# Kernel optimization log

Measured on AMD Instinct MI355X. Metric: run time of the kernel, lower is better.

Reference implementation:

```python
import jax, jax.numpy as jnp
import numpy as np

DIM = 1152
HEADS = 9
MID = 256
B, N = 8, 1024


def _conprefix(x, dw, db, uw, ub):
    # torch Linear: y = x @ W.T + b
    kv = jnp.tanh(x @ dw.T + db) @ uw.T + ub  # [B, N, 2*dim]
    q = jnp.zeros(kv.shape[:2] + (DIM,), kv.dtype)
    return jnp.concatenate([q, kv], axis=-1)  # [B, N, 3*dim]


def setup_inputs() -> dict:
    key = jax.random.key(0)
    ks = jax.random.split(key, 12)
    s = 0.02
    return {
        "x": jax.random.normal(ks[0], (B, N, DIM), dtype=jnp.float32),
        "Wqkv": jax.random.normal(ks[1], (3 * DIM, DIM), dtype=jnp.float32) * s,
        "Wproj": jax.random.normal(ks[2], (DIM, DIM), dtype=jnp.float32) * s,
        "bproj": jax.random.normal(ks[3], (DIM,), dtype=jnp.float32) * s,
        "down_w": jax.random.normal(ks[4], (MID, DIM), dtype=jnp.float32) * s,
        "down_b": jax.random.normal(ks[5], (MID,), dtype=jnp.float32) * s,
        "up_w": jax.random.normal(ks[6], (2 * DIM, MID), dtype=jnp.float32) * s,
        "up_b": jax.random.normal(ks[7], (2 * DIM,), dtype=jnp.float32) * s,
        "pdown_w": jax.random.normal(ks[8], (MID, DIM), dtype=jnp.float32) * s,
        "pdown_b": jax.random.normal(ks[9], (MID,), dtype=jnp.float32) * s,
        "pup_w": jax.random.normal(ks[10], (2 * DIM, MID), dtype=jnp.float32) * s,
        "pup_b": jax.random.normal(ks[11], (2 * DIM,), dtype=jnp.float32) * s,
        "task": 5,
    }


def reference(x, Wqkv, Wproj, bproj, down_w, down_b, up_w, up_b,
              pdown_w, pdown_b, pup_w, pup_b, task):
    b, n, c = x.shape
    hd = c // HEADS
    scale = hd ** (-0.5)
    qkv = x @ Wqkv.T  # [B, N, 3C] (qkv_bias=False)
    task_prefix_tensor = None
    if task <= 3:
        pass
    elif task == 4:
        qkv = qkv + _conprefix(x, down_w, down_b, up_w, up_b)
        task_prefix_tensor = down_w
    else:
        qkv = (qkv + _conprefix(x, pdown_w, pdown_b, pup_w, pup_b)
                   + _conprefix(x, down_w, down_b, up_w, up_b))
        task_prefix_tensor = down_w
    qkv = qkv.reshape(b, n, 3, HEADS, hd).transpose(2, 0, 3, 1, 4)  # [3,B,H,N,hd]
    q, k, v = qkv[0], qkv[1], qkv[2]
    attn = jax.nn.softmax(jnp.einsum('bhqd,bhkd->bhqk', q, k) * scale, axis=-1)
    out = jnp.einsum('bhqk,bhkd->bhqd', attn, v)  # [B,H,N,hd]
    out = out.transpose(0, 2, 1, 3).reshape(b, n, c)
    out = out @ Wproj.T + bproj
    return (out, task_prefix_tensor)
```

## Files before the change

kernel.cpp:

```cpp
#include <hip/hip_runtime.h>
#include <math.h>

namespace {

typedef unsigned short u16;
typedef __attribute__((ext_vector_type(8))) short short8;
typedef __attribute__((ext_vector_type(4))) float f32x4;
typedef __attribute__((ext_vector_type(16))) float f32x16;

constexpr int kDim   = 1152;
constexpr int kHeads = 9;
constexpr int kMid   = 256;
constexpr int kB     = 8;
constexpr int kN     = 1024;
constexpr int kM     = kB * kN;
constexpr int kQS    = 3584;
constexpr float kCexp  = 0.12753837360881433f;

__device__ __forceinline__ u16 f2bf(float f) {
    unsigned u = __builtin_bit_cast(unsigned, f);
    return (u16)((u + 0x7FFFu + ((u >> 16) & 1u)) >> 16);
}
__device__ __forceinline__ float bf2f(u16 h) {
    unsigned u = ((unsigned)h) << 16;
    return __builtin_bit_cast(float, u);
}

__device__ __forceinline__ void gload_lds16(const void* g, void* l) {
    __builtin_amdgcn_global_load_lds(
        (const __attribute__((address_space(1))) unsigned int*)g,
        (__attribute__((address_space(3))) unsigned int*)l,
        16, 0, 0);
}

__device__ __forceinline__ unsigned cvtpk(float a, float b) {
    unsigned r;
    asm volatile("v_cvt_pk_bf16_f32 %0, %1, %2" : "=v"(r) : "v"(a), "v"(b));
    return r;
}

__device__ __forceinline__ void halfswap(unsigned& x, unsigned& y, bool hihalf) {
    const unsigned xs = (unsigned)__shfl_xor((int)x, 32);
    const unsigned ys = (unsigned)__shfl_xor((int)y, 32);
    const unsigned nx = hihalf ? ys : x;
    const unsigned ny = hihalf ? y : xs;
    x = nx; y = ny;
}

__device__ __forceinline__ short8 build_pfrag(float p0, float p1, float p2, float p3,
                                              float p4, float p5, float p6, float p7,
                                              bool hihalf) {
    unsigned x1 = cvtpk(p0, p1), y1 = cvtpk(p4, p5);
    unsigned x2 = cvtpk(p2, p3), y2 = cvtpk(p6, p7);
    halfswap(x1, y1, hihalf);
    halfswap(x2, y2, hihalf);
    union { unsigned u[4]; short8 s; } pk;
    pk.u[0] = x1; pk.u[1] = x2; pk.u[2] = y1; pk.u[3] = y2;
    return pk.s;
}

constexpr int R0 = 2359296;
constexpr int R1 = R0 + 995328;
constexpr int R2 = R1 + 331776;
constexpr int R3 = R2 + 73728;
constexpr int R4 = R3 + 73728;
constexpr int R5 = R4 + 147456;
constexpr int R6 = R5 + 147456;
constexpr int R7 = R6 + 512;
constexpr int R8 = R7 + 2304;
constexpr int kQPart = 331776;
constexpr int kPrepGrid = R8 / 256;

__global__ __launch_bounds__(256)
void prep_all(const float* __restrict__ x, const float* __restrict__ Wqkv,
              const float* __restrict__ Wproj,
              const float* __restrict__ down_w, const float* __restrict__ pdown_w,
              const float* __restrict__ up_w, const float* __restrict__ pup_w,
              const float* __restrict__ down_b, const float* __restrict__ pdown_b,
              const float* __restrict__ up_b, const float* __restrict__ pup_b,
              const int* __restrict__ task,
              u16* __restrict__ xb, u16* __restrict__ wqkvb, u16* __restrict__ wprjb,
              u16* __restrict__ wdownb, u16* __restrict__ wupb,
              float* __restrict__ bd, float* __restrict__ bu)
{
    const int i = blockIdx.x * blockDim.x + threadIdx.x;
    auto cvt4s = [](const float* s, int j, float sc) {
        const float4 v = reinterpret_cast<const float4*>(s)[j];
        ushort4 o;
        o.x = f2bf(v.x * sc); o.y = f2bf(v.y * sc);
        o.z = f2bf(v.z * sc); o.w = f2bf(v.w * sc);
        return o;
    };
    if (i < R0) {
        reinterpret_cast<ushort4*>(xb)[i] = cvt4s(x, i, 1.f);
    } else if (i < R1) {
        const int j = i - R0;
        const float sc = (j < kQPart) ? kCexp : 1.f;
        reinterpret_cast<ushort4*>(wqkvb)[j] = cvt4s(Wqkv, j, sc);
    } else if (i < R2) {
        reinterpret_cast<ushort4*>(wprjb)[i - R1] = cvt4s(Wproj, i - R1, 1.f);
    } else if (i < R3) {
        reinterpret_cast<ushort4*>(wdownb)[i - R2] = cvt4s(down_w, i - R2, 1.f);
    } else if (i < R4) {
        reinterpret_cast<ushort4*>(wdownb)[73728 + (i - R3)] = cvt4s(pdown_w, i - R3, 1.f);
    } else if (i < R5) {
        const int j = i - R4, r = j >> 6, c = j & 63;
        reinterpret_cast<ushort4*>(wupb)[r * 128 + c] = cvt4s(up_w, j, 1.f);
    } else if (i < R6) {
        const int j = i - R5, r = j >> 6, c = j & 63;
        reinterpret_cast<ushort4*>(wupb)[r * 128 + 64 + c] = cvt4s(pup_w, j, 1.f);
    } else if (i < R7) {
        const int j = i - R6;
        bd[j] = (j < 256) ? down_b[j] : pdown_b[j - 256];
    } else {
        const int j = i - R7;
        bu[j] = up_b[j] + ((*task >= 5) ? pup_b[j] : 0.f);
    }
}

template<bool ACCUM, bool BIAS>
__global__ __launch_bounds__(512, 2)
void gemm8p(const u16* __restrict__ A, const u16* __restrict__ Bw,
            const float* __restrict__ bias, u16* __restrict__ C,
            int K, int lda, int ldb, int ldc)
{
    extern __shared__ char lds[];

    const int tid  = threadIdx.x;
    const int lane = tid & 63;
    const int wid  = tid >> 6;
    const int wm   = wid >> 2;
    const int wn   = wid & 3;
    const int bm   = blockIdx.x * 256;
    const int bn   = blockIdx.y * 256;
    const int l15  = lane & 15;
    const int kq   = lane >> 4;

    int srow[4], scol[4], sdst[4];
#pragma unroll
    for (int i = 0; i < 4; ++i) {
        const int id = i * 512 + tid;
        srow[i] = id >> 3;
        const int s = id & 7;
        scol[i] = (s ^ (srow[i] & 7)) * 8;
        sdst[i] = (i * 512 + wid * 64) * 16;
    }

    auto stage_pair = [&](int buf, int kt, int i) {
        const u16* ag = A  + (size_t)bm * lda + kt * 64;
        const u16* bg = Bw + (size_t)bn * ldb + kt * 64;
        gload_lds16(ag + (size_t)srow[i] * lda + scol[i], lds + buf * 32768 + sdst[i]);
        gload_lds16(bg + (size_t)srow[i] * ldb + scol[i], lds + 65536 + buf * 32768 + sdst[i]);
    };

    f32x4 acc[8][4] = {};
    const int nt = K >> 6;

#pragma unroll
    for (int i = 0; i < 4; ++i) stage_pair(0, 0, i);

    for (int t = 0; t < nt; ++t) {
        const char* Ab = lds + (t & 1) * 32768;
        const char* Bb = lds + 65536 + (t & 1) * 32768;
        const bool nxt = (t + 1 < nt);
        const int nb = (t + 1) & 1;

        short8 af[4], bf[4];

        auto rdA = [&](int mh, int ks) {
#pragma unroll
            for (int mi = 0; mi < 4; ++mi) {
                const int row = wm * 128 + mh * 64 + mi * 16 + l15;
                af[mi] = *reinterpret_cast<const short8*>(
                    Ab + row * 128 + (((ks * 4 + kq) ^ (row & 7)) * 16));
            }
        };
        auto rdB = [&](int ks) {
#pragma unroll
            for (int ni = 0; ni < 4; ++ni) {
                const int row = wn * 64 + ni * 16 + l15;
                bf[ni] = *reinterpret_cast<const short8*>(
                    Bb + row * 128 + (((ks * 4 + kq) ^ (row & 7)) * 16));
            }
        };
        auto mfma16 = [&](int mh) {
            asm volatile("s_waitcnt lgkmcnt(0)" ::: "memory");
            __builtin_amdgcn_sched_barrier(0);
            __builtin_amdgcn_s_setprio(1);
#pragma unroll
            for (int mi = 0; mi < 4; ++mi)
#pragma unroll
                for (int ni = 0; ni < 4; ++ni)
                    acc[mh * 4 + mi][ni] = __builtin_amdgcn_mfma_f32_16x16x32_bf16(
                        af[mi], bf[ni], acc[mh * 4 + mi][ni], 0, 0, 0);
            __builtin_amdgcn_s_setprio(0);
            asm volatile("" ::: "memory");
            __builtin_amdgcn_s_barrier();
            asm volatile("" ::: "memory");
        };

        if (nxt) { stage_pair(nb, t + 1, 0); stage_pair(nb, t + 1, 1); }
        if (nxt) asm volatile("s_waitcnt vmcnt(4)" ::: "memory");
        else     asm volatile("s_waitcnt vmcnt(0)" ::: "memory");
        __builtin_amdgcn_sched_barrier(0);
        __builtin_amdgcn_s_barrier();
        asm volatile("" ::: "memory");
        rdB(0); rdA(0, 0);
        mfma16(0);

        if (nxt) { stage_pair(nb, t + 1, 2); stage_pair(nb, t + 1, 3); }
        rdA(1, 0);
        mfma16(1);

        rdB(1); rdA(0, 1);
        mfma16(0);

        rdA(1, 1);
        mfma16(1);
    }

#pragma unroll
    for (int mg = 0; mg < 8; ++mg) {
#pragma unroll
        for (int ni = 0; ni < 4; ++ni) {
            const int col = bn + wn * 64 + ni * 16 + l15;
            const float bv = BIAS ? bias[col] : 0.f;
#pragma unroll
            for (int r = 0; r < 4; ++r) {
                const int row = bm + wm * 128 + mg * 16 + kq * 4 + r;
                float v = acc[mg][ni][r] + bv;
                u16* cp = C + (size_t)row * ldc + col;
                if (ACCUM) v += bf2f(*cp);
                *cp = f2bf(v);
            }
        }
    }
}

template<bool TANH, bool ACCUM, bool BIAS, bool OUT_BF16, bool KSEL>
__global__ __launch_bounds__(256)
void gemm_mfma(const u16* __restrict__ A, const u16* __restrict__ Bw,
               const float* __restrict__ bias, void* __restrict__ Cv,
               int K, int lda, int ldb, int ldc,
               const int* __restrict__ taskp, int mintask)
{
    if (taskp != nullptr && *taskp < mintask) return;
    if (KSEL && *taskp < 5) K = 256;

    __shared__ u16 As[2][128 * 64];
    __shared__ u16 Bs[2][128 * 64];

    const int tid  = threadIdx.x;
    const int lane = tid & 63;
    const int wv   = tid >> 6;
    const int wr   = (wv >> 1) * 64;
    const int wc   = (wv & 1) * 64;
    const int bm   = blockIdx.x * 128;
    const int bn   = blockIdx.y * 128;

    f32x4 acc[4][4] = {};

    const int srow = tid >> 3;
    const int sslt = tid & 7;

    auto stage = [&](int buf, int k0) {
        const u16* ab = A  + (size_t)bm * lda + k0;
        const u16* bb = Bw + (size_t)bn * ldb + k0;
#pragma unroll
        for (int i = 0; i < 4; ++i) {
            const int row = i * 32 + srow;
            gload_lds16(ab + (size_t)row * lda + sslt * 8,
                        (char*)&As[buf][0] + (i * 256 + (tid & 192)) * 16);
        }
#pragma unroll
        for (int i = 0; i < 4; ++i) {
            const int row = i * 32 + srow;
            gload_lds16(bb + (size_t)row * ldb + sslt * 8,
                        (char*)&Bs[buf][0] + (i * 256 + (tid & 192)) * 16);
        }
    };

    stage(0, 0);
    const int nk = K >> 6;
    for (int kt = 0; kt < nk; ++kt) {
        __syncthreads();
        if (kt + 1 < nk) stage((kt + 1) & 1, (kt + 1) * 64);
        const u16* as = &As[kt & 1][0];
        const u16* bs = &Bs[kt & 1][0];
#pragma unroll
        for (int ks = 0; ks < 2; ++ks) {
            short8 af[4], bf[4];
#pragma unroll
            for (int mi = 0; mi < 4; ++mi) {
                const int row = wr + mi * 16 + (lane & 15);
                af[mi] = *reinterpret_cast<const short8*>(as + row * 64 + ks * 32 + (lane >> 4) * 8);
            }
#pragma unroll
            for (int ni = 0; ni < 4; ++ni) {
                const int row = wc + ni * 16 + (lane & 15);
                bf[ni] = *reinterpret_cast<const short8*>(bs + row * 64 + ks * 32 + (lane >> 4) * 8);
            }
#pragma unroll
            for (int mi = 0; mi < 4; ++mi)
#pragma unroll
                for (int ni = 0; ni < 4; ++ni)
                    acc[mi][ni] = __builtin_amdgcn_mfma_f32_16x16x32_bf16(
                        af[mi], bf[ni], acc[mi][ni], 0, 0, 0);
        }
    }

#pragma unroll
    for (int mi = 0; mi < 4; ++mi) {
#pragma unroll
        for (int ni = 0; ni < 4; ++ni) {
            const int col = bn + wc + ni * 16 + (lane & 15);
            const float bv = BIAS ? bias[col] : 0.f;
#pragma unroll
            for (int r = 0; r < 4; ++r) {
                const int row = bm + wr + mi * 16 + (lane >> 4) * 4 + r;
                float v = acc[mi][ni][r] + bv;
                if (TANH) v = tanhf(v);
                if (OUT_BF16) {
                    u16* cp = (u16*)Cv + (size_t)row * ldc + col;
                    if (ACCUM) v += bf2f(*cp);
                    *cp = f2bf(v);
                } else {
                    float* cp = (float*)Cv + (size_t)row * ldc + col;
                    if (ACCUM) v += *cp;
                    *cp = v;
                }
            }
        }
    }
}

__global__ __launch_bounds__(256)
void transpose_v(const u16* __restrict__ qkv, u16* __restrict__ vt)
{
    __shared__ u16 t[64][136];
    const int bh = blockIdx.x, b = bh / kHeads, h = bh - b * kHeads;
    const int n0 = blockIdx.y * 64;
    const int tid = threadIdx.x;
#pragma unroll
    for (int it = 0; it < 4; ++it) {
        const int I = it * 256 + tid, tok = I >> 4, s = I & 15;
        *reinterpret_cast<short8*>(&t[tok][s * 8]) =
            *reinterpret_cast<const short8*>(
                qkv + (size_t)(b * kN + n0 + tok) * kQS + 2304 + h * 128 + s * 8);
    }
    __syncthreads();
#pragma unroll
    for (int it = 0; it < 8; ++it) {
        const int I = it * 256 + tid;
        const int d = I >> 4, tk = (I & 15) * 4;
        ushort4 v;
        v.x = t[tk + 0][d]; v.y = t[tk + 1][d];
        v.z = t[tk + 2][d]; v.w = t[tk + 3][d];
        *reinterpret_cast<ushort4*>(vt + (size_t)(bh * 128 + d) * kN + n0 + tk) = v;
    }
}

__global__ __launch_bounds__(256)
void attn_mfma(const u16* __restrict__ qkv, const u16* __restrict__ vt,
               u16* __restrict__ out)
{
    __shared__ u16 Ks[64 * 128];
    __shared__ u16 Vs[128 * 64];

    const int bh = blockIdx.x, b = bh / kHeads, h = bh - b * kHeads;
    const int tid = threadIdx.x, lane = tid & 63, wv = tid >> 6;
    const int lo5 = lane & 31;
    const bool hihalf = (lane >= 32);
    const int hi = hihalf ? 1 : 0;
    const int q0 = blockIdx.y * 128 + wv * 32;

    const u16* qp = qkv + (size_t)(b * kN + q0 + lo5) * kQS + h * 128;
    short8 qf[8];
#pragma unroll
    for (int f = 0; f < 8; ++f)
        qf[f] = *reinterpret_cast<const short8*>(qp + f * 16 + hi * 8);

    int koff[4], voff[4];
#pragma unroll
    for (int j = 0; j < 4; ++j) {
        const int I = (wv * 4 + j) * 64 + lane;
        const int tok = I >> 4, s = I & 15;
        koff[j] = tok * kQS + ((s ^ (tok & 7)) * 8);
        const int d = I >> 3, sv = I & 7;
        voff[j] = d * kN + ((sv ^ (d & 7)) * 8);
    }
    const u16* kbase = qkv + (size_t)b * kN * kQS + kDim + h * 128;
    const u16* vbase = vt + (size_t)bh * 128 * kN;

    f32x16 o[4] = {};
    float l = 0.f;

    for (int kt = 0; kt < kN; kt += 64) {
        __syncthreads();
#pragma unroll
        for (int j = 0; j < 4; ++j)
            gload_lds16(kbase + (size_t)kt * kQS + koff[j], (char*)Ks + (wv * 4 + j) * 1024);
#pragma unroll
        for (int j = 0; j < 4; ++j)
            gload_lds16(vbase + kt + voff[j], (char*)Vs + (wv * 4 + j) * 1024);
        __syncthreads();

        f32x16 s0 = {}, s1 = {};
        __builtin_amdgcn_s_setprio(1);
#pragma unroll
        for (int f = 0; f < 8; ++f) {
            const int c = (f * 2 + hi) * 16;
            const int swz = (lo5 & 7) << 4;
            const short8 ka = *reinterpret_cast<const short8*>(
                (const char*)Ks + lo5 * 256 + (c ^ swz));
            const short8 kb = *reinterpret_cast<const short8*>(
                (const char*)Ks + (lo5 + 32) * 256 + (c ^ swz));
            s0 = __builtin_amdgcn_mfma_f32_32x32x16_bf16(ka, qf[f], s0, 0, 0, 0);
            s1 = __builtin_amdgcn_mfma_f32_32x32x16_bf16(kb, qf[f], s1, 0, 0, 0);
        }
        __builtin_amdgcn_s_setprio(0);

        float rsum = 0.f;
#pragma unroll
        for (int r = 0; r < 16; ++r) { s0[r] = exp2f(s0[r]); rsum += s0[r]; }
#pragma unroll
        for (int r = 0; r < 16; ++r) { s1[r] = exp2f(s1[r]); rsum += s1[r]; }
        rsum += __shfl_xor(rsum, 32);
        l += rsum;

        short8 pf[4];
        pf[0] = build_pfrag(s0[0], s0[1], s0[2], s0[3], s0[4], s0[5], s0[6], s0[7], hihalf);
        pf[1] = build_pfrag(s0[8], s0[9], s0[10], s0[11], s0[12], s0[13], s0[14], s0[15], hihalf);
        pf[2] = build_pfrag(s1[0], s1[1], s1[2], s1[3], s1[4], s1[5], s1[6], s1[7], hihalf);
        pf[3] = build_pfrag(s1[8], s1[9], s1[10], s1[11], s1[12], s1[13], s1[14], s1[15], hihalf);

        __builtin_amdgcn_s_setprio(1);
#pragma unroll
        for (int dt = 0; dt < 4; ++dt) {
            const int drow = dt * 32 + lo5;
            const int swz = (lo5 & 7) << 4;
#pragma unroll
            for (int c = 0; c < 4; ++c) {
                const int col = (c * 2 + hi) * 16;
                const short8 va = *reinterpret_cast<const short8*>(
                    (const char*)Vs + drow * 128 + (col ^ swz));
                o[dt] = __builtin_amdgcn_mfma_f32_32x32x16_bf16(va, pf[c], o[dt], 0, 0, 0);
            }
        }
        __builtin_amdgcn_s_setprio(0);
    }

    const float inv = 1.f / l;
    u16* op = out + (size_t)(b * kN + q0 + lo5) * kDim + h * 128;
#pragma unroll
    for (int dt = 0; dt < 4; ++dt) {
#pragma unroll
        for (int rg = 0; rg < 4; ++rg) {
            const int d0 = dt * 32 + rg * 8 + hi * 4;
            ushort4 v;
            v.x = f2bf(o[dt][rg * 4 + 0] * inv);
            v.y = f2bf(o[dt][rg * 4 + 1] * inv);
            v.z = f2bf(o[dt][rg * 4 + 2] * inv);
            v.w = f2bf(o[dt][rg * 4 + 3] * inv);
            *reinterpret_cast<ushort4*>(op + d0) = v;
        }
    }
}

}

extern "C" void kernel_launch(void* const* d_in, const int* in_sizes, int n_in,
                              void* d_out, int out_size, void* d_ws, size_t ws_size,
                              hipStream_t stream)
{
    const float* x       = (const float*)d_in[0];
    const float* Wqkv    = (const float*)d_in[1];
    const float* Wproj   = (const float*)d_in[2];
    const float* bproj   = (const float*)d_in[3];
    const float* down_w  = (const float*)d_in[4];
    const float* down_b  = (const float*)d_in[5];
    const float* up_w    = (const float*)d_in[6];
    const float* up_b    = (const float*)d_in[7];
    const float* pdown_w = (const float*)d_in[8];
    const float* pdown_b = (const float*)d_in[9];
    const float* pup_w   = (const float*)d_in[10];
    const float* pup_b   = (const float*)d_in[11];
    const int*   task    = (const int*)d_in[12];

    u16* xb_vt  = (u16*)d_ws;
    u16* wqkvb  = xb_vt  + (size_t)kM * kDim;
    u16* wprjb  = wqkvb  + (size_t)kQS * kDim;
    u16* wdownb = wprjb  + (size_t)kDim * kDim;
    u16* wupb   = wdownb + (size_t)512 * kDim;
    u16* h12    = wupb   + (size_t)2304 * 512;
    u16* qkvb   = h12    + (size_t)kM * 512;
    u16* aob    = qkvb   + (size_t)kM * kQS;
    float* bd   = (float*)(aob + (size_t)kM * kDim);
    float* bu   = bd + 512;
    float* out  = (float*)d_out;
    u16* xb = xb_vt;
    u16* vt = xb_vt;

    prep_all<<<kPrepGrid, 256, 0, stream>>>(
        x, Wqkv, Wproj, down_w, pdown_w, up_w, pup_w,
        down_b, pdown_b, up_b, pup_b, task,
        xb, wqkvb, wprjb, wdownb, wupb, bd, bu);

    hipFuncSetAttribute(reinterpret_cast<const void*>(&gemm8p<false, false>),
                        hipFuncAttributeMaxDynamicSharedMemorySize, 131072);

    gemm_mfma<true, false, true, true, false><<<dim3(kM / 128, 4), 256, 0, stream>>>(
        xb, wdownb, bd, h12, kDim, kDim, kDim, 512, nullptr, 0);
    gemm8p<false, false><<<dim3(kM / 256, kQS / 256), 512, 131072, stream>>>(
        xb, wqkvb, nullptr, qkvb, kDim, kDim, kDim, kQS);
    gemm_mfma<false, true, true, true, true><<<dim3(kM / 128, 18), 256, 0, stream>>>(
        h12, wupb, bu, qkvb + kDim, 512, 512, 512, kQS, task, 4);

    transpose_v<<<dim3(kB * kHeads, kN / 64), 256, 0, stream>>>(qkvb, vt);

    attn_mfma<<<dim3(kB * kHeads, kN / 128), 256, 0, stream>>>(qkvb, vt, aob);

    gemm_mfma<false, false, true, false, false><<<dim3(kM / 128, 9), 256, 0, stream>>>(
        aob, wprjb, bproj, out, kDim, kDim, kDim, kDim, nullptr, 0);

    hipMemcpyAsync(out + (size_t)kM * kDim, down_w,
                   (size_t)kMid * kDim * sizeof(float),
                   hipMemcpyDeviceToDevice, stream);
}
```

Before: 339.6 us.

## Split attention key range across wave pairs and merge partial outputs via LDS

```diff
diff --git a/kernel.cpp b/kernel.cpp
--- a/kernel.cpp
+++ b/kernel.cpp
@@ -364,15 +364,17 @@
 void attn_mfma(const u16* __restrict__ qkv, const u16* __restrict__ vt,
                u16* __restrict__ out)
 {
-    __shared__ u16 Ks[64 * 128];
-    __shared__ u16 Vs[128 * 64];
+    __shared__ u16 Ks[2][32 * 128];
+    __shared__ u16 Vs[2][128 * 32];
 
     const int bh = blockIdx.x, b = bh / kHeads, h = bh - b * kHeads;
     const int tid = threadIdx.x, lane = tid & 63, wv = tid >> 6;
     const int lo5 = lane & 31;
     const bool hihalf = (lane >= 32);
     const int hi = hihalf ? 1 : 0;
-    const int q0 = blockIdx.y * 128 + wv * 32;
+    const int qh = wv >> 1;
+    const int kh = wv & 1;
+    const int q0 = blockIdx.y * 64 + qh * 32;
 
     const u16* qp = qkv + (size_t)(b * kN + q0 + lo5) * kQS + h * 128;
     short8 qf[8];
@@ -380,14 +382,14 @@
     for (int f = 0; f < 8; ++f)
         qf[f] = *reinterpret_cast<const short8*>(qp + f * 16 + hi * 8);
 
-    int koff[4], voff[4];
-#pragma unroll
-    for (int j = 0; j < 4; ++j) {
-        const int I = (wv * 4 + j) * 64 + lane;
+    int koff[2], voff[2];
+#pragma unroll
+    for (int j = 0; j < 2; ++j) {
+        const int I = j * 256 + tid;
         const int tok = I >> 4, s = I & 15;
         koff[j] = tok * kQS + ((s ^ (tok & 7)) * 8);
-        const int d = I >> 3, sv = I & 7;
-        voff[j] = d * kN + ((sv ^ (d & 7)) * 8);
+        const int d = I >> 2, sv = I & 3;
+        voff[j] = d * kN + ((sv ^ (d & 3)) * 8);
     }
     const u16* kbase = qkv + (size_t)b * kN * kQS + kDim + h * 128;
     const u16* vbase = vt + (size_t)bh * 128 * kN;
@@ -395,74 +397,97 @@
     f32x16 o[4] = {};
     float l = 0.f;
 
-    for (int kt = 0; kt < kN; kt += 64) {
+    for (int t = 0; t < 16; ++t) {
         __syncthreads();
 #pragma unroll
-        for (int j = 0; j < 4; ++j)
-            gload_lds16(kbase + (size_t)kt * kQS + koff[j], (char*)Ks + (wv * 4 + j) * 1024);
-#pragma unroll
-        for (int j = 0; j < 4; ++j)
-            gload_lds16(vbase + kt + voff[j], (char*)Vs + (wv * 4 + j) * 1024);
+        for (int hh = 0; hh < 2; ++hh) {
+            const int kt = hh * 512 + t * 32;
+#pragma unroll
+            for (int j = 0; j < 2; ++j) {
+                gload_lds16(kbase + (size_t)kt * kQS + koff[j],
+                            (char*)&Ks[hh][0] + (j * 256 + wv * 64) * 16);
+                gload_lds16(vbase + kt + voff[j],
+                            (char*)&Vs[hh][0] + (j * 256 + wv * 64) * 16);
+            }
+        }
         __syncthreads();
 
-        f32x16 s0 = {}, s1 = {};
+        const char* ks = (const char*)&Ks[kh][0];
+        const char* vs = (const char*)&Vs[kh][0];
+
+        f32x16 s0 = {};
         __builtin_amdgcn_s_setprio(1);
 #pragma unroll
         for (int f = 0; f < 8; ++f) {
-            const int c = (f * 2 + hi) * 16;
-            const int swz = (lo5 & 7) << 4;
             const short8 ka = *reinterpret_cast<const short8*>(
-                (const char*)Ks + lo5 * 256 + (c ^ swz));
-            const short8 kb = *reinterpret_cast<const short8*>(
-                (const char*)Ks + (lo5 + 32) * 256 + (c ^ swz));
+                ks + lo5 * 256 + (((f * 2 + hi) * 16) ^ ((lo5 & 7) << 4)));
             s0 = __builtin_amdgcn_mfma_f32_32x32x16_bf16(ka, qf[f], s0, 0, 0, 0);
-            s1 = __builtin_amdgcn_mfma_f32_32x32x16_bf16(kb, qf[f], s1, 0, 0, 0);
         }
         __builtin_amdgcn_s_setprio(0);
 
         float rsum = 0.f;
 #pragma unroll
         for (int r = 0; r < 16; ++r) { s0[r] = exp2f(s0[r]); rsum += s0[r]; }
-#pragma unroll
-        for (int r = 0; r < 16; ++r) { s1[r] = exp2f(s1[r]); rsum += s1[r]; }
         rsum += __shfl_xor(rsum, 32);
         l += rsum;
 
-        short8 pf[4];
+        short8 pf[2];
         pf[0] = build_pfrag(s0[0], s0[1], s0[2], s0[3], s0[4], s0[5], s0[6], s0[7], hihalf);
         pf[1] = build_pfrag(s0[8], s0[9], s0[10], s0[11], s0[12], s0[13], s0[14], s0[15], hihalf);
-        pf[2] = build_pfrag(s1[0], s1[1], s1[2], s1[3], s1[4], s1[5], s1[6], s1[7], hihalf);
-        pf[3] = build_pfrag(s1[8], s1[9], s1[10], s1[11], s1[12], s1[13], s1[14], s1[15], hihalf);
 
         __builtin_amdgcn_s_setprio(1);
 #pragma unroll
         for (int dt = 0; dt < 4; ++dt) {
             const int drow = dt * 32 + lo5;
-            const int swz = (lo5 & 7) << 4;
-#pragma unroll
-            for (int c = 0; c < 4; ++c) {
-                const int col = (c * 2 + hi) * 16;
+#pragma unroll
+            for (int c = 0; c < 2; ++c) {
                 const short8 va = *reinterpret_cast<const short8*>(
-                    (const char*)Vs + drow * 128 + (col ^ swz));
+                    vs + drow * 64 + (((c * 2 + hi) * 16) ^ ((drow & 3) << 4)));
                 o[dt] = __builtin_amdgcn_mfma_f32_32x32x16_bf16(va, pf[c], o[dt], 0, 0, 0);
             }
         }
         __builtin_amdgcn_s_setprio(0);
     }
 
-    const float inv = 1.f / l;
-    u16* op = out + (size_t)(b * kN + q0 + lo5) * kDim + h * 128;
-#pragma unroll
-    for (int dt = 0; dt < 4; ++dt) {
-#pragma unroll
-        for (int rg = 0; rg < 4; ++rg) {
-            const int d0 = dt * 32 + rg * 8 + hi * 4;
-            ushort4 v;
-            v.x = f2bf(o[dt][rg * 4 + 0] * inv);
-            v.y = f2bf(o[dt][rg * 4 + 1] * inv);
-            v.z = f2bf(o[dt][rg * 4 + 2] * inv);
-            v.w = f2bf(o[dt][rg * 4 + 3] * inv);
-            *reinterpret_cast<ushort4*>(op + d0) = v;
+    __syncthreads();
+    char* exch = (char*)&Ks[0][0];
+    float* ls  = (float*)&Vs[0][0];
+    if (kh == 1) {
+#pragma unroll
+        for (int dt = 0; dt < 4; ++dt) {
+#pragma unroll
+            for (int rg = 0; rg < 4; ++rg) {
+                const int kb = (dt * 4 + rg) * 8;
+                ushort4 w;
+                w.x = f2bf(o[dt][rg * 4 + 0]);
+                w.y = f2bf(o[dt][rg * 4 + 1]);
+                w.z = f2bf(o[dt][rg * 4 + 2]);
+                w.w = f2bf(o[dt][rg * 4 + 3]);
+                *reinterpret_cast<ushort4*>(
+                    exch + qh * 8192 + lane * 128 + (kb ^ ((lane & 7) << 3))) = w;
+            }
+        }
+        if (!hihalf) ls[qh * 32 + lo5] = l;
+    }
+    __syncthreads();
+    if (kh == 0) {
+        const float inv = 1.f / (l + ls[qh * 32 + lo5]);
+        u16* op = out + (size_t)(b * kN + q0 + lo5) * kDim + h * 128;
+#pragma unroll
+        for (int dt = 0; dt < 4; ++dt) {
+#pragma unroll
+            for (int rg = 0; rg < 4; ++rg) {
+                const int kb = (dt * 4 + rg) * 8;
+                const ushort4 pv = *reinterpret_cast<const ushort4*>(
+                    exch + qh * 8192 + lane * 128 + (kb ^ ((lane & 7) << 3)));
+                const int d0 = dt * 32 + rg * 8 + hi * 4;
+                ushort4 v;
+                v.x = f2bf((o[dt][rg * 4 + 0] + bf2f(pv.x)) * inv);
+                v.y = f2bf((o[dt][rg * 4 + 1] + bf2f(pv.y)) * inv);
+                v.z = f2bf((o[dt][rg * 4 + 2] + bf2f(pv.z)) * inv);
+                v.w = f2bf((o[dt][rg * 4 + 3] + bf2f(pv.w)) * inv);
+                *reinterpret_cast<ushort4*>(op + d0) = v;
+            }
         }
     }
 }
@@ -518,7 +543,7 @@
 
     transpose_v<<<dim3(kB * kHeads, kN / 64), 256, 0, stream>>>(qkvb, vt);
 
-    attn_mfma<<<dim3(kB * kHeads, kN / 128), 256, 0, stream>>>(qkvb, vt, aob);
+    attn_mfma<<<dim3(kB * kHeads, kN / 64), 256, 0, stream>>>(qkvb, vt, aob);
 
     gemm_mfma<false, false, true, false, false><<<dim3(kM / 128, 9), 256, 0, stream>>>(
         aob, wprjb, bproj, out, kDim, kDim, kDim, kDim, nullptr, 0);
```

Measured after the change: 330.4 us (median of 2 runs). -2.7%, faster.
